# Kernel optimization log

Hardware: AMD Instinct MI355X
Metric: run time of the kernel (lower is better)

Reference implementation:

```python
import jax, jax.numpy as jnp
import numpy as np

# Config derived from init_kwargs
DIM = 256
DSTATE = 64
DCONV = 3
HEADDIM = 64
CHUNK = 256
NGROUPS = 1
DINNER = int(2.0 * DIM)                 # 512
NHEADS = DINNER // HEADDIM              # 8
CONVDIM = DINNER + 2 * NGROUPS * DSTATE  # 640 (x, B, C share the depthwise conv)
DPROJ = 2 * DINNER + 2 * NGROUPS * DSTATE + NHEADS  # z + xBC + dt


def setup_inputs() -> dict:
    key = jax.random.key(0)
    ks = jax.random.split(key, 8)
    B, H, W = 8, 64, 64
    return dict(
        x=jax.random.normal(ks[0], (B, DIM, H, W), jnp.float32),
        ln_w=jnp.ones((DIM,), jnp.float32),
        ln_b=jnp.zeros((DIM,), jnp.float32),
        in_proj_w=jax.random.normal(ks[1], (DPROJ, DIM), jnp.float32) * 0.02,
        conv_w=jax.random.normal(ks[2], (CONVDIM, 1, DCONV, DCONV), jnp.float32) * 0.1,
        conv_b=jnp.zeros((CONVDIM,), jnp.float32),
        A_log=jnp.log(jax.random.uniform(ks[3], (NHEADS,), jnp.float32, 1.0, 16.0)),
        D=jnp.ones((NHEADS,), jnp.float32),
        dt_bias=jax.random.uniform(ks[4], (NHEADS,), jnp.float32, -2.0, 0.0),
        rms_w=jnp.ones((DINNER,), jnp.float32),
        out_proj_w=jax.random.normal(ks[5], (DIM, DINNER), jnp.float32) * 0.02,
    )


def _ssd(X, dA, Bm, Cm, chunk):
    """Mamba2 SSD chunked parallel scan.
    X:  (b, l, h, p)  inputs already multiplied by dt
    dA: (b, l, h)     dt * A (negative)
    Bm, Cm: (b, l, h, n)
    """
    b, l, h, p = X.shape
    n = Bm.shape[-1]
    c = l // chunk
    q = chunk
    Xc = X.reshape(b, c, q, h, p)
    Bc = Bm.reshape(b, c, q, h, n)
    Cc = Cm.reshape(b, c, q, h, n)
    Ac = dA.reshape(b, c, q, h).transpose(0, 3, 1, 2)            # (b,h,c,q)
    Acs = jnp.cumsum(Ac, axis=-1)                                # (b,h,c,q)
    # intra-chunk (diagonal blocks): causal decay matrix L
    tri = jnp.tril(jnp.ones((q, q), bool))
    Ldec = jnp.where(tri, jnp.exp(Acs[..., :, None] - Acs[..., None, :]), 0.0)
    Y_diag = jnp.einsum('bcqhn,bcshn,bhcqs,bcshp->bcqhp', Cc, Bc, Ldec, Xc)
    # per-chunk final states
    decay_states = jnp.exp(Acs[..., -1:] - Acs)                  # (b,h,c,q)
    states = jnp.einsum('bcqhn,bhcq,bcqhp->bchpn', Bc, decay_states, Xc)
    # inter-chunk recurrence (segment-sum over chunk totals)
    A_last = jnp.pad(Acs[..., -1], ((0, 0), (0, 0), (1, 0)))     # (b,h,c+1)
    ccs = jnp.cumsum(A_last, axis=-1)
    tric = jnp.tril(jnp.ones((c + 1, c + 1), bool))
    decay_chunk = jnp.where(tric, jnp.exp(ccs[..., :, None] - ccs[..., None, :]), 0.0)
    states0 = jnp.concatenate([jnp.zeros_like(states[:, :1]), states], axis=1)
    prev = jnp.einsum('bhzc,bchpn->bzhpn', decay_chunk, states0)[:, :-1]
    # contribution of carried-in state (off-diagonal blocks)
    Y_off = jnp.einsum('bcqhn,bchpn,bhcq->bcqhp', Cc, prev, jnp.exp(Acs))
    return (Y_diag + Y_off).reshape(b, l, h, p)


def _forward(x, ln_w, ln_b, in_proj_w, conv_w, conv_b, A_log, D, dt_bias, rms_w, out_proj_w):
    Bn, Cd, Hh, Ww = x.shape
    L = Hh * Ww
    # LayerNorm over channel dim (channel-first LayerNorm2d)
    mu = jnp.mean(x, axis=1, keepdims=True)
    var = jnp.mean((x - mu) ** 2, axis=1, keepdims=True)
    xn = (x - mu) * jax.lax.rsqrt(var + 1e-5)
    xn = xn * ln_w[None, :, None, None] + ln_b[None, :, None, None]
    # input projection (1x1): -> z | xBC | dt
    zxbcdt = jnp.einsum('bchw,dc->bdhw', xn, in_proj_w)
    z = zxbcdt[:, :DINNER]
    xBC = zxbcdt[:, DINNER:DINNER + CONVDIM]
    dt = zxbcdt[:, DINNER + CONVDIM:]                            # (b, nheads, H, W)
    # depthwise 2D conv + SiLU on xBC
    xBC = jax.lax.conv_general_dilated(
        xBC, conv_w, (1, 1), 'SAME',
        dimension_numbers=('NCHW', 'OIHW', 'NCHW'), feature_group_count=CONVDIM)
    xBC = jax.nn.silu(xBC + conv_b[None, :, None, None])
    # flatten spatial -> sequence, channel-last
    def to_seq(t):
        return t.reshape(Bn, t.shape[1], L).transpose(0, 2, 1)
    xBC, dt, z = to_seq(xBC), to_seq(dt), to_seq(z)
    xs = xBC[..., :DINNER].reshape(Bn, L, NHEADS, HEADDIM)
    Bg = xBC[..., DINNER:DINNER + NGROUPS * DSTATE].reshape(Bn, L, NGROUPS, DSTATE)
    Cg = xBC[..., DINNER + NGROUPS * DSTATE:].reshape(Bn, L, NGROUPS, DSTATE)
    hpg = NHEADS // NGROUPS
    Bm = jnp.repeat(Bg, hpg, axis=2)
    Cm = jnp.repeat(Cg, hpg, axis=2)
    dt = jax.nn.softplus(dt + dt_bias[None, None, :])            # (b, L, nheads)
    A = -jnp.exp(A_log)
    y = _ssd(xs * dt[..., None], dt * A[None, None, :], Bm, Cm, CHUNK)
    y = y + D[None, None, :, None] * xs                          # skip connection
    y = y.reshape(Bn, L, DINNER)
    # gated RMSNorm: norm(y * silu(z)) * w
    y = y * jax.nn.silu(z)
    y = y * jax.lax.rsqrt(jnp.mean(y * y, axis=-1, keepdims=True) + 1e-5) * rms_w
    out = jnp.einsum('bld,cd->blc', y, out_proj_w)
    out = out.transpose(0, 2, 1).reshape(Bn, Cd, Hh, Ww)
    return x + out                                               # residual


def reference(x, ln_w, ln_b, in_proj_w, conv_w, conv_b, A_log, D, dt_bias, rms_w, out_proj_w):
    return _forward(x, ln_w, ln_b, in_proj_w, conv_w, conv_b, A_log, D, dt_bias, rms_w, out_proj_w)
```

## Files before the change

kernel.cpp:

```cpp
#include <hip/hip_runtime.h>
#include <hip/hip_bf16.h>
#include <math.h>

#define DIMC   256
#define LSP    4096
#define BATCH  8
#define DINNER 512
#define NHEADS 8
#define HEADDIM 64
#define DSTATE 64
#define CONVDIM 640
#define DPROJ  1160
#define MPAD   1280
#define CHUNK  256
#define NCHUNK 16

typedef unsigned short u16;
typedef __attribute__((ext_vector_type(8))) unsigned short u16x8;
typedef __attribute__((ext_vector_type(8))) short s16x8;
typedef __attribute__((ext_vector_type(4))) float f32x4;

#define MFMA16(a,b,c) __builtin_amdgcn_mfma_f32_16x16x32_bf16((s16x8)(a),(s16x8)(b),(c),0,0,0)

__device__ __forceinline__ float bf2f(u16 u){ return __uint_as_float(((unsigned int)u)<<16); }
__device__ __forceinline__ u16 f2bf(float f){
  unsigned int x = __float_as_uint(f);
  unsigned int r = (x + 0x7fffu + ((x>>16)&1u)) >> 16;
  return (u16)r;
}
__device__ __forceinline__ float softplusf(float x){ return (x > 20.f) ? x : __logf(1.f + __expf(x)); }
__device__ __forceinline__ float siluf(float x){ return x * __builtin_amdgcn_rcpf(1.f + __expf(-x)); }

__global__ void convert_w(const float* __restrict__ src, u16* __restrict__ dst,
                          int total, int valid){
  int i = blockIdx.x*256 + threadIdx.x;
  if (i >= total) return;
  dst[i] = (i < valid) ? f2bf(src[i]) : (u16)0;
}

__global__ void convert_w_rms(const float* __restrict__ src, const float* __restrict__ rmsw,
                              u16* __restrict__ dst){
  int i = blockIdx.x*256 + threadIdx.x;
  if (i >= DIMC*DINNER) return;
  dst[i] = f2bf(src[i] * rmsw[i & (DINNER-1)]);
}

__global__ void ln_kernel(const float* __restrict__ X, const float* __restrict__ lnw,
                          const float* __restrict__ lnb, u16* __restrict__ XNT) {
  int pos = blockIdx.x*256 + threadIdx.x;
  int b = pos >> 12, l = pos & (LSP-1);
  const float* xb = X + ((size_t)b*DIMC)*LSP + l;
  float sum=0.f, sq=0.f;
  for (int c=0;c<DIMC;c++){ float v=xb[(size_t)c*LSP]; sum+=v; sq+=v*v; }
  float mu = sum*(1.f/DIMC);
  float var = sq*(1.f/DIMC) - mu*mu;
  float rs = rsqrtf(var + 1e-5f);
  u16* ob = XNT + ((size_t)(b*LSP + l))*DIMC;
  for (int c0=0;c0<DIMC;c0+=8){
    u16x8 v8;
    #pragma unroll
    for(int j=0;j<8;j++){
      float v = xb[(size_t)(c0+j)*LSP];
      v8[j] = f2bf((v-mu)*rs*lnw[c0+j] + lnb[c0+j]);
    }
    *(u16x8*)&ob[c0] = v8;
  }
}

__global__ __launch_bounds__(256,2) void gemm_in_fused(
    const u16* __restrict__ W, const u16* __restrict__ XNT,
    u16* __restrict__ ZT, u16* __restrict__ XBC, u16* __restrict__ DT){
  __shared__ u16 Xs[128][264];
  __shared__ u16 Ws[128][32];
  int tid=threadIdx.x, w=tid>>6, lane=tid&63, l15=lane&15, quad=lane>>4;
  int n0=blockIdx.x*128, mh=blockIdx.y, b=blockIdx.z;
  {
    const u16* src = XNT + ((size_t)(b*LSP + n0))*DIMC;
    #pragma unroll
    for (int i=0;i<16;i++){
      int g = i*256 + tid;
      int row = g>>5, c8 = (g&31)*8;
      *(u16x8*)&Xs[row][c8] = *(const u16x8*)&src[(size_t)row*DIMC + c8];
    }
  }
  for (int pti=0; pti<5; pti++){
    int ptg = mh*5 + pti;
    int m0 = ptg*128;
    f32x4 acc[4][4];
    #pragma unroll
    for(int i=0;i<4;i++)
      #pragma unroll
      for(int j=0;j<4;j++) acc[i][j]=(f32x4){0.f,0.f,0.f,0.f};
    for (int k0=0;k0<DIMC;k0+=32){
      __syncthreads();
      {
        int ch = tid*2;
        int r = ch>>2, o=(ch&3)*8;
        *(u16x8*)&Ws[r][o] = *(const u16x8*)&W[(size_t)(m0+r)*DIMC + k0 + o];
        ch++; r = ch>>2; o=(ch&3)*8;
        *(u16x8*)&Ws[r][o] = *(const u16x8*)&W[(size_t)(m0+r)*DIMC + k0 + o];
      }
      __syncthreads();
      u16x8 af[4], bfr[4];
      if (ptg < 4){
        #pragma unroll
        for(int mt=0;mt<4;mt++) af[mt] = *(const u16x8*)&Xs[(w>>1)*64+mt*16+l15][k0+quad*8];
        #pragma unroll
        for(int nt=0;nt<4;nt++) bfr[nt] = *(const u16x8*)&Ws[(w&1)*64+nt*16+l15][quad*8];
      } else {
        #pragma unroll
        for(int mt=0;mt<4;mt++) af[mt] = *(const u16x8*)&Ws[(w>>1)*64+mt*16+l15][quad*8];
        #pragma unroll
        for(int nt=0;nt<4;nt++) bfr[nt] = *(const u16x8*)&Xs[(w&1)*64+nt*16+l15][k0+quad*8];
      }
      #pragma unroll
      for(int mt=0;mt<4;mt++)
        #pragma unroll
        for(int nt=0;nt<4;nt++)
          acc[mt][nt]=MFMA16(af[mt],bfr[nt],acc[mt][nt]);
    }
    if (ptg < 4){
      #pragma unroll
      for(int mt=0;mt<4;mt++)
        #pragma unroll
        for(int nt=0;nt<4;nt++)
          #pragma unroll
          for(int r=0;r<4;r++){
            int lrow = n0 + (w>>1)*64 + mt*16 + quad*4 + r;
            int dcol = m0 + (w&1)*64 + nt*16 + l15;
            ZT[((size_t)b*LSP + lrow)*DINNER + dcol] = f2bf(acc[mt][nt][r]);
          }
    } else {
      #pragma unroll
      for(int mt=0;mt<4;mt++)
        #pragma unroll
        for(int nt=0;nt<4;nt++)
          #pragma unroll
          for(int r=0;r<4;r++){
            int prow = m0 + (w>>1)*64 + mt*16 + quad*4 + r;
            if (prow>=DPROJ) continue;
            int col = n0 + (w&1)*64 + nt*16 + l15;
            u16 v = f2bf(acc[mt][nt][r]);
            if (prow<DINNER+CONVDIM)  XBC[((size_t)b*CONVDIM+(prow-DINNER))*LSP+col]=v;
            else                      DT[((size_t)b*NHEADS+(prow-DINNER-CONVDIM))*LSP+col]=v;
          }
    }
  }
}

__global__ void gemm_out_mfma(const u16* __restrict__ A, const u16* __restrict__ Bm,
                              const float* __restrict__ Res, float* __restrict__ Out){
  __shared__ u16 As[128][32];
  __shared__ u16 Bs[128][32];
  __shared__ float rinv[128];
  int tid=threadIdx.x, w=tid>>6, lane=tid&63, l15=lane&15, quad=lane>>4;
  int b=blockIdx.z, m0=blockIdx.y*128, n0=blockIdx.x*128;
  const u16* Bb = Bm + ((size_t)b*LSP + n0)*DINNER;
  f32x4 acc[4][4];
  #pragma unroll
  for(int i=0;i<4;i++)
    #pragma unroll
    for(int j=0;j<4;j++) acc[i][j] = (f32x4){0.f,0.f,0.f,0.f};
  float sqacc = 0.f;
  for (int k0=0;k0<DINNER;k0+=32){
    __syncthreads();
    {
      int ch = tid*2;
      int r = ch>>2, o=(ch&3)*8;
      *(u16x8*)&As[r][o] = *(const u16x8*)&A[(size_t)(m0+r)*DINNER + k0 + o];
      u16x8 bv = *(const u16x8*)&Bb[(size_t)r*DINNER + k0 + o];
      *(u16x8*)&Bs[r][o] = bv;
      #pragma unroll
      for(int j=0;j<8;j++){ float f=bf2f(bv[j]); sqacc += f*f; }
      ch++; r = ch>>2; o=(ch&3)*8;
      *(u16x8*)&As[r][o] = *(const u16x8*)&A[(size_t)(m0+r)*DINNER + k0 + o];
      u16x8 bv2 = *(const u16x8*)&Bb[(size_t)r*DINNER + k0 + o];
      *(u16x8*)&Bs[r][o] = bv2;
      #pragma unroll
      for(int j=0;j<8;j++){ float f=bf2f(bv2[j]); sqacc += f*f; }
    }
    __syncthreads();
    u16x8 af[4], bfr[4];
    #pragma unroll
    for(int mt=0;mt<4;mt++) af[mt] = *(const u16x8*)&As[(w>>1)*64+mt*16+l15][quad*8];
    #pragma unroll
    for(int nt=0;nt<4;nt++) bfr[nt] = *(const u16x8*)&Bs[(w&1)*64+nt*16+l15][quad*8];
    #pragma unroll
    for(int mt=0;mt<4;mt++)
      #pragma unroll
      for(int nt=0;nt<4;nt++)
        acc[mt][nt]=MFMA16(af[mt],bfr[nt],acc[mt][nt]);
  }
  {
    float tot = sqacc + __shfl_xor(sqacc, 1, 64);
    if ((tid&1)==0) rinv[tid>>1] = rsqrtf(tot*(1.f/DINNER) + 1e-5f);
  }
  __syncthreads();
  #pragma unroll
  for(int mt=0;mt<4;mt++)
    #pragma unroll
    for(int nt=0;nt<4;nt++){
      float rv = rinv[(w&1)*64 + nt*16 + l15];
      #pragma unroll
      for(int r=0;r<4;r++){
        int row = m0 + (w>>1)*64 + mt*16 + quad*4 + r;
        int col = n0 + (w&1)*64 + nt*16 + l15;
        size_t oi = ((size_t)b*DIMC+row)*LSP+col;
        Out[oi] = acc[mt][nt][r]*rv + Res[oi];
      }
    }
}

__global__ void conv_kernel(u16* __restrict__ XBC, const float* __restrict__ CW,
                            const float* __restrict__ CB){
  int ch = blockIdx.x, b = blockIdx.y, tid = threadIdx.x;
  __shared__ float plane[66*66];
  u16* base = XBC + ((size_t)b*CONVDIM + ch)*LSP;
  for (int idx=tid; idx<66*66; idx+=256){
    int yy = idx/66 - 1, xx = idx%66 - 1;
    float v = 0.f;
    if (yy>=0 && yy<64 && xx>=0 && xx<64) v = bf2f(base[yy*64+xx]);
    plane[idx] = v;
  }
  float wg[9];
  #pragma unroll
  for (int t=0;t<9;t++) wg[t] = CW[ch*9+t];
  float bias = CB[ch];
  __syncthreads();
  for (int r=0;r<16;r++){
    int pix = tid + r*256;
    int y = pix>>6, x = pix&63;
    float s=0.f;
    #pragma unroll
    for(int dy=0;dy<3;dy++)
      #pragma unroll
      for(int dx=0;dx<3;dx++) s += plane[(y+dy)*66 + x+dx]*wg[dy*3+dx];
    base[pix] = f2bf(siluf(s + bias));
  }
}

__global__ void ssd_pre_kernel(const u16* __restrict__ DT, const float* __restrict__ A_log,
                               const float* __restrict__ dt_bias, float* __restrict__ ACS,
                               float* __restrict__ DTV, float* __restrict__ DASUM){
  int c=blockIdx.x, h=blockIdx.y, b=blockIdx.z, tid=threadIdx.x;
  __shared__ float acs[CHUNK];
  size_t base = ((size_t)b*NHEADS+h)*LSP + c*CHUNK + tid;
  float raw = bf2f(DT[base]);
  float dtv = softplusf(raw + dt_bias[h]);
  float Ah = -__expf(A_log[h]);
  acs[tid] = dtv*Ah;
  __syncthreads();
  for(int o=1;o<256;o<<=1){
    float add=(tid>=o)?acs[tid-o]:0.f;
    __syncthreads(); acs[tid]+=add; __syncthreads();
  }
  ACS[base] = acs[tid];
  DTV[base] = dtv;
  if (tid==CHUNK-1) DASUM[((size_t)b*NHEADS+h)*NCHUNK+c] = acs[tid];
}

__global__ __launch_bounds__(256,4) void ssd_states_mfma(
    const float* __restrict__ ACS, const float* __restrict__ DTV,
    const float* __restrict__ DASUM, const u16* __restrict__ XBC,
    float* __restrict__ STATES){
  int c=blockIdx.x, h=blockIdx.y, b=blockIdx.z;
  int tid=threadIdx.x, w=tid>>6, lane=tid&63, l15=lane&15, quad=lane>>4;
  __shared__ float wdt[CHUNK];
  __shared__ u16 Xw[64][136];
  __shared__ u16 Bn[64][136];
  {
    size_t base = ((size_t)b*NHEADS+h)*LSP + c*CHUNK + tid;
    float atot = DASUM[((size_t)b*NHEADS+h)*NCHUNK+c];
    wdt[tid] = DTV[base]*__expf(atot - ACS[base]);
  }
  __syncthreads();
  f32x4 acc[4];
  #pragma unroll
  for(int i=0;i<4;i++) acc[i] = (f32x4){0.f,0.f,0.f,0.f};
  size_t cb = (size_t)c*CHUNK;
  for(int th=0; th<2; th++){
    __syncthreads();
    {
      int n=tid&63, q4=tid>>6;
      const u16* Xg = XBC + ((size_t)b*CONVDIM + h*HEADDIM + n)*LSP + cb + th*128;
      const u16* Bg = XBC + ((size_t)b*CONVDIM + DINNER + n)*LSP + cb + th*128;
      #pragma unroll
      for(int i=0;i<4;i++){
        int o = q4*32+i*8;
        u16x8 v = *(const u16x8*)&Xg[o];
        u16x8 wv;
        #pragma unroll
        for(int j=0;j<8;j++) wv[j]=f2bf(bf2f(v[j])*wdt[th*128+o+j]);
        *(u16x8*)&Xw[n][o]=wv;
        *(u16x8*)&Bn[n][o] = *(const u16x8*)&Bg[o];
      }
    }
    __syncthreads();
    #pragma unroll
    for(int k8=0;k8<4;k8++){
      u16x8 a = *(const u16x8*)&Xw[w*16+l15][k8*32+quad*8];
      #pragma unroll
      for(int nt=0;nt<4;nt++){
        u16x8 bb = *(const u16x8*)&Bn[nt*16+l15][k8*32+quad*8];
        acc[nt]=MFMA16(a,bb,acc[nt]);
      }
    }
  }
  float* dst = STATES + (((size_t)b*NHEADS+h)*NCHUNK+c)*4096;
  #pragma unroll
  for(int nt=0;nt<4;nt++)
    #pragma unroll
    for(int r=0;r<4;r++)
      dst[(w*16+quad*4+r)*64 + nt*16+l15] = acc[nt][r];
}

__global__ void ssd_scan_kernel(const float* __restrict__ STATES, const float* __restrict__ DASUM,
                                u16* __restrict__ PREVB){
  int g = blockIdx.x, h = blockIdx.y, b = blockIdx.z, tid = threadIdx.x;
  int e = g*256 + tid;
  size_t hb = (size_t)b*NHEADS + h;
  size_t base = hb*NCHUNK*4096 + e;
  float s = 0.f;
  for (int cc=0;cc<NCHUNK;cc++){
    PREVB[base + (size_t)cc*4096] = f2bf(s);
    s = s*__expf(DASUM[hb*NCHUNK + cc]) + STATES[base + (size_t)cc*4096];
  }
}

__global__ __launch_bounds__(256,7) void ssd_y_mfma(
    const float* __restrict__ ACS, const float* __restrict__ DTV,
    const u16* __restrict__ XBC, const float* __restrict__ Dp,
    const u16* __restrict__ PREVB, const u16* __restrict__ ZT,
    u16* __restrict__ YG){
  int h = blockIdx.x, bx = blockIdx.y, b = blockIdx.z;
  int c = bx>>2, tb = 3-(bx&3);
  int tid=threadIdx.x, w=tid>>6, lane=tid&63, l15=lane&15, quad=lane>>4;
  __shared__ float acs[CHUNK];
  __shared__ float dtv[CHUNK];
  __shared__ u16 BP[64][72];
  __shared__ u16 Xsb[64][72];
  {
    size_t base = ((size_t)b*NHEADS+h)*LSP + c*CHUNK + tid;
    acs[tid] = ACS[base];
    dtv[tid] = DTV[base];
  }
  u16x8 ca0, ca1;
  {
    const u16* Cbase = XBC + ((size_t)b*CONVDIM + DINNER + DSTATE)*LSP
                     + (size_t)c*CHUNK + tb*64 + w*16 + l15;
    #pragma unroll
    for(int j=0;j<8;j++){
      ca0[j] = Cbase[(size_t)(quad*8+j)*LSP];
      ca1[j] = Cbase[(size_t)(32+quad*8+j)*LSP];
    }
  }
  __syncthreads();
  f32x4 Yd[4], Yo[4];
  #pragma unroll
  for(int i=0;i<4;i++){ Yd[i]=(f32x4){0.f,0.f,0.f,0.f}; Yo[i]=(f32x4){0.f,0.f,0.f,0.f}; }
  {
    const u16* Pg = PREVB + (((size_t)b*NHEADS+h)*NCHUNK + c)*4096;
    #pragma unroll
    for(int pt=0;pt<4;pt++){
      u16x8 b0 = *(const u16x8*)&Pg[(pt*16+l15)*64 + quad*8];
      u16x8 b1 = *(const u16x8*)&Pg[(pt*16+l15)*64 + 32 + quad*8];
      Yo[pt]=MFMA16(ca0,b0,Yo[pt]);
      Yo[pt]=MFMA16(ca1,b1,Yo[pt]);
    }
  }
  int tloc = tb*64 + w*16 + quad*4;
  float acst[4];
  #pragma unroll
  for(int r=0;r<4;r++) acst[r] = acs[tloc+r];
  float Dh = Dp[h];
  for(int sb=0; sb<=tb; sb++){
    __syncthreads();
    {
      int n=tid&63, q4=tid>>6;
      const u16* Bg = XBC + ((size_t)b*CONVDIM + DINNER + n)*LSP + (size_t)c*CHUNK + sb*64;
      #pragma unroll
      for(int i=0;i<2;i++){
        u16x8 v = *(const u16x8*)&Bg[q4*16+i*8];
        #pragma unroll
        for(int j=0;j<8;j++) BP[q4*16+i*8+j][n]=v[j];
      }
      const u16* Xg = XBC + ((size_t)b*CONVDIM + h*HEADDIM + n)*LSP + (size_t)c*CHUNK + sb*64;
      #pragma unroll
      for(int i=0;i<2;i++){
        int o = q4*16+i*8;
        *(u16x8*)&Xsb[n][o] = *(const u16x8*)&Xg[o];
      }
    }
    __syncthreads();
    f32x4 S[4];
    #pragma unroll
    for(int st=0;st<4;st++){
      S[st]=(f32x4){0.f,0.f,0.f,0.f};
      u16x8 b0 = *(const u16x8*)&BP[st*16+l15][quad*8];
      u16x8 b1 = *(const u16x8*)&BP[st*16+l15][32+quad*8];
      S[st]=MFMA16(ca0,b0,S[st]);
      S[st]=MFMA16(ca1,b1,S[st]);
    }
    __syncthreads();
    if (sb < tb){
      #pragma unroll
      for(int st=0;st<4;st++){
        int s = sb*64 + st*16 + l15;
        float as = acs[s], dv = dtv[s];
        #pragma unroll
        for(int r=0;r<4;r++)
          BP[w*16+quad*4+r][st*16+l15] = f2bf(S[st][r]*__expf(acst[r]-as)*dv);
      }
    } else {
      #pragma unroll
      for(int st=0;st<4;st++){
        int s = sb*64 + st*16 + l15;
        float as = acs[s], dv = dtv[s];
        #pragma unroll
        for(int r=0;r<4;r++){
          int t = tloc + r;
          float pv;
          if (s < t)       pv = S[st][r]*__expf(acst[r]-as)*dv;
          else if (s == t) pv = S[st][r]*dv + Dh;
          else             pv = 0.f;
          BP[w*16+quad*4+r][st*16+l15] = f2bf(pv);
        }
      }
    }
    u16x8 p0 = *(const u16x8*)&BP[w*16+l15][quad*8];
    u16x8 p1 = *(const u16x8*)&BP[w*16+l15][32+quad*8];
    #pragma unroll
    for(int pt=0;pt<4;pt++){
      u16x8 x0 = *(const u16x8*)&Xsb[pt*16+l15][quad*8];
      u16x8 x1 = *(const u16x8*)&Xsb[pt*16+l15][32+quad*8];
      Yd[pt]=MFMA16(p0,x0,Yd[pt]);
      Yd[pt]=MFMA16(p1,x1,Yd[pt]);
    }
  }
  float eat[4];
  #pragma unroll
  for(int r=0;r<4;r++) eat[r] = __expf(acst[r]);
  size_t lbase = (size_t)b*LSP + c*CHUNK + tb*64;
  #pragma unroll
  for(int pt=0;pt<4;pt++){
    #pragma unroll
    for(int r=0;r<4;r++){
      int tl = w*16 + quad*4 + r;
      int p = pt*16 + l15;
      float y = Yd[pt][r] + eat[r]*Yo[pt][r];
      size_t oi = (lbase + tl)*DINNER + h*HEADDIM + p;
      float zv = bf2f(ZT[oi]);
      YG[oi] = f2bf(y * siluf(zv));
    }
  }
}

extern "C" void kernel_launch(void* const* d_in, const int* in_sizes, int n_in,
                              void* d_out, int out_size, void* d_ws, size_t ws_size,
                              hipStream_t stream) {
  const float* x     = (const float*)d_in[0];
  const float* lnw   = (const float*)d_in[1];
  const float* lnb   = (const float*)d_in[2];
  const float* inpw  = (const float*)d_in[3];
  const float* convw = (const float*)d_in[4];
  const float* convb = (const float*)d_in[5];
  const float* alog  = (const float*)d_in[6];
  const float* Dp    = (const float*)d_in[7];
  const float* dtbi  = (const float*)d_in[8];
  const float* rmsw  = (const float*)d_in[9];
  const float* outw  = (const float*)d_in[10];
  float* out = (float*)d_out;

  char* ws = (char*)d_ws;
  size_t off = 0;
  auto alloc = [&](size_t bytes)->void*{ void* p = ws+off; off += (bytes+255)&~(size_t)255; return p; };
  u16*   WPIN   = (u16*)  alloc((size_t)MPAD*DIMC*2);
  u16*   WPOUT  = (u16*)  alloc((size_t)DIMC*DINNER*2);
  char*  RA     = (char*) alloc((size_t)BATCH*NHEADS*NCHUNK*4096*4);
  u16*   XNT    = (u16*)RA;
  float* STATES = (float*)RA;
  u16*   ZT     = (u16*)  alloc((size_t)BATCH*LSP*DINNER*2);
  u16*   XBC    = (u16*)  alloc((size_t)BATCH*CONVDIM*LSP*2);
  u16*   DTb    = (u16*)  alloc((size_t)BATCH*NHEADS*LSP*2);
  u16*   PREVB  = (u16*)  alloc((size_t)BATCH*NHEADS*NCHUNK*4096*2);
  float* DASUM  = (float*)alloc((size_t)BATCH*NHEADS*NCHUNK*4);
  float* ACS    = (float*)alloc((size_t)BATCH*NHEADS*LSP*4);
  float* DTV    = (float*)alloc((size_t)BATCH*NHEADS*LSP*4);
  u16*   YG     = (u16*)  alloc((size_t)BATCH*LSP*DINNER*2);

  convert_w<<<(MPAD*DIMC+255)/256,256,0,stream>>>(inpw, WPIN, MPAD*DIMC, DPROJ*DIMC);
  convert_w_rms<<<(DIMC*DINNER+255)/256,256,0,stream>>>(outw, rmsw, WPOUT);
  ln_kernel<<<dim3(BATCH*LSP/256),256,0,stream>>>(x,lnw,lnb,XNT);
  gemm_in_fused<<<dim3(LSP/128,2,BATCH),256,0,stream>>>(WPIN, XNT, ZT, XBC, DTb);
  conv_kernel<<<dim3(CONVDIM,BATCH),256,0,stream>>>(XBC, convw, convb);
  ssd_pre_kernel<<<dim3(NCHUNK,NHEADS,BATCH),256,0,stream>>>(DTb, alog, dtbi, ACS, DTV, DASUM);
  ssd_states_mfma<<<dim3(NCHUNK,NHEADS,BATCH),256,0,stream>>>(ACS,DTV,DASUM,XBC,STATES);
  ssd_scan_kernel<<<dim3(16,NHEADS,BATCH),256,0,stream>>>(STATES,DASUM,PREVB);
  ssd_y_mfma<<<dim3(NHEADS,NCHUNK*4,BATCH),256,0,stream>>>(ACS,DTV,XBC,Dp,PREVB,ZT,YG);
  gemm_out_mfma<<<dim3(LSP/128,DIMC/128,BATCH),256,0,stream>>>(WPOUT, YG, x, out);
}
```

Before: 346.9 us.

## Process two heads per block in SSD output kernel with vectorized epilogue

Each ssd_y_mfma block now handles two heads, so the shared B/C score matrix (C·B^T) and the C and B tile loads are computed once and reused for both heads, halving the grid. The separate P buffer removes one barrier per sub-block. The epilogue stages Y in shared memory and writes YG with 16-byte vector loads and stores, where before each element was a scattered scalar access. In exchange, register and LDS use roughly double, so launch bounds drop to 3 blocks per CU and there are fewer blocks to hide latency.

After: 318.8 us. -8.1%, faster.

```diff
diff --git a/kernel.cpp b/kernel.cpp
--- a/kernel.cpp
+++ b/kernel.cpp
@@ -327,22 +327,26 @@
   }
 }
 
-__global__ __launch_bounds__(256,7) void ssd_y_mfma(
+__global__ __launch_bounds__(256,3) void ssd_y_mfma(
     const float* __restrict__ ACS, const float* __restrict__ DTV,
     const u16* __restrict__ XBC, const float* __restrict__ Dp,
     const u16* __restrict__ PREVB, const u16* __restrict__ ZT,
     u16* __restrict__ YG){
-  int h = blockIdx.x, bx = blockIdx.y, b = blockIdx.z;
+  int hp = blockIdx.x, bx = blockIdx.y, b = blockIdx.z;
+  int h0 = hp*2;
   int c = bx>>2, tb = 3-(bx&3);
   int tid=threadIdx.x, w=tid>>6, lane=tid&63, l15=lane&15, quad=lane>>4;
-  __shared__ float acs[CHUNK];
-  __shared__ float dtv[CHUNK];
-  __shared__ u16 BP[64][72];
-  __shared__ u16 Xsb[64][72];
-  {
-    size_t base = ((size_t)b*NHEADS+h)*LSP + c*CHUNK + tid;
-    acs[tid] = ACS[base];
-    dtv[tid] = DTV[base];
+  __shared__ float acs2[2][CHUNK];
+  __shared__ float dtv2[2][CHUNK];
+  __shared__ u16 Bs[64][72];
+  __shared__ u16 Xs[2][64][72];
+  __shared__ u16 Ps[2][64][72];
+  {
+    size_t base0 = ((size_t)b*NHEADS+h0)*LSP + c*CHUNK + tid;
+    acs2[0][tid] = ACS[base0];
+    dtv2[0][tid] = DTV[base0];
+    acs2[1][tid] = ACS[base0 + LSP];
+    dtv2[1][tid] = DTV[base0 + LSP];
   }
   u16x8 ca0, ca1;
   {
@@ -355,24 +359,29 @@
     }
   }
   __syncthreads();
-  f32x4 Yd[4], Yo[4];
-  #pragma unroll
-  for(int i=0;i<4;i++){ Yd[i]=(f32x4){0.f,0.f,0.f,0.f}; Yo[i]=(f32x4){0.f,0.f,0.f,0.f}; }
-  {
-    const u16* Pg = PREVB + (((size_t)b*NHEADS+h)*NCHUNK + c)*4096;
+  f32x4 Yd[2][4], Yo[2][4];
+  #pragma unroll
+  for(int hh=0;hh<2;hh++)
+    #pragma unroll
+    for(int i=0;i<4;i++){ Yd[hh][i]=(f32x4){0.f,0.f,0.f,0.f}; Yo[hh][i]=(f32x4){0.f,0.f,0.f,0.f}; }
+  #pragma unroll
+  for(int hh=0;hh<2;hh++){
+    const u16* Pg = PREVB + (((size_t)b*NHEADS+h0+hh)*NCHUNK + c)*4096;
     #pragma unroll
     for(int pt=0;pt<4;pt++){
       u16x8 b0 = *(const u16x8*)&Pg[(pt*16+l15)*64 + quad*8];
       u16x8 b1 = *(const u16x8*)&Pg[(pt*16+l15)*64 + 32 + quad*8];
-      Yo[pt]=MFMA16(ca0,b0,Yo[pt]);
-      Yo[pt]=MFMA16(ca1,b1,Yo[pt]);
+      Yo[hh][pt]=MFMA16(ca0,b0,Yo[hh][pt]);
+      Yo[hh][pt]=MFMA16(ca1,b1,Yo[hh][pt]);
     }
   }
   int tloc = tb*64 + w*16 + quad*4;
-  float acst[4];
-  #pragma unroll
-  for(int r=0;r<4;r++) acst[r] = acs[tloc+r];
-  float Dh = Dp[h];
+  float acst[2][4];
+  #pragma unroll
+  for(int hh=0;hh<2;hh++)
+    #pragma unroll
+    for(int r=0;r<4;r++) acst[hh][r] = acs2[hh][tloc+r];
+  float DhA[2] = { Dp[h0], Dp[h0+1] };
   for(int sb=0; sb<=tb; sb++){
     __syncthreads();
     {
@@ -382,13 +391,16 @@
       for(int i=0;i<2;i++){
         u16x8 v = *(const u16x8*)&Bg[q4*16+i*8];
         #pragma unroll
-        for(int j=0;j<8;j++) BP[q4*16+i*8+j][n]=v[j];
-      }
-      const u16* Xg = XBC + ((size_t)b*CONVDIM + h*HEADDIM + n)*LSP + (size_t)c*CHUNK + sb*64;
-      #pragma unroll
-      for(int i=0;i<2;i++){
-        int o = q4*16+i*8;
-        *(u16x8*)&Xsb[n][o] = *(const u16x8*)&Xg[o];
+        for(int j=0;j<8;j++) Bs[q4*16+i*8+j][n]=v[j];
+      }
+      #pragma unroll
+      for(int hh=0;hh<2;hh++){
+        const u16* Xg = XBC + ((size_t)b*CONVDIM + (h0+hh)*HEADDIM + n)*LSP + (size_t)c*CHUNK + sb*64;
+        #pragma unroll
+        for(int i=0;i<2;i++){
+          int o = q4*16+i*8;
+          *(u16x8*)&Xs[hh][n][o] = *(const u16x8*)&Xg[o];
+        }
       }
     }
     __syncthreads();
@@ -396,61 +408,85 @@
     #pragma unroll
     for(int st=0;st<4;st++){
       S[st]=(f32x4){0.f,0.f,0.f,0.f};
-      u16x8 b0 = *(const u16x8*)&BP[st*16+l15][quad*8];
-      u16x8 b1 = *(const u16x8*)&BP[st*16+l15][32+quad*8];
+      u16x8 b0 = *(const u16x8*)&Bs[st*16+l15][quad*8];
+      u16x8 b1 = *(const u16x8*)&Bs[st*16+l15][32+quad*8];
       S[st]=MFMA16(ca0,b0,S[st]);
       S[st]=MFMA16(ca1,b1,S[st]);
     }
-    __syncthreads();
-    if (sb < tb){
-      #pragma unroll
-      for(int st=0;st<4;st++){
-        int s = sb*64 + st*16 + l15;
-        float as = acs[s], dv = dtv[s];
-        #pragma unroll
-        for(int r=0;r<4;r++)
-          BP[w*16+quad*4+r][st*16+l15] = f2bf(S[st][r]*__expf(acst[r]-as)*dv);
-      }
-    } else {
-      #pragma unroll
-      for(int st=0;st<4;st++){
-        int s = sb*64 + st*16 + l15;
-        float as = acs[s], dv = dtv[s];
-        #pragma unroll
-        for(int r=0;r<4;r++){
-          int t = tloc + r;
-          float pv;
-          if (s < t)       pv = S[st][r]*__expf(acst[r]-as)*dv;
-          else if (s == t) pv = S[st][r]*dv + Dh;
-          else             pv = 0.f;
-          BP[w*16+quad*4+r][st*16+l15] = f2bf(pv);
+    #pragma unroll
+    for(int hh=0;hh<2;hh++){
+      float Dh = DhA[hh];
+      if (sb < tb){
+        #pragma unroll
+        for(int st=0;st<4;st++){
+          int s = sb*64 + st*16 + l15;
+          float as = acs2[hh][s], dv = dtv2[hh][s];
+          #pragma unroll
+          for(int r=0;r<4;r++)
+            Ps[hh][w*16+quad*4+r][st*16+l15] = f2bf(S[st][r]*__expf(acst[hh][r]-as)*dv);
         }
-      }
-    }
-    u16x8 p0 = *(const u16x8*)&BP[w*16+l15][quad*8];
-    u16x8 p1 = *(const u16x8*)&BP[w*16+l15][32+quad*8];
-    #pragma unroll
-    for(int pt=0;pt<4;pt++){
-      u16x8 x0 = *(const u16x8*)&Xsb[pt*16+l15][quad*8];
-      u16x8 x1 = *(const u16x8*)&Xsb[pt*16+l15][32+quad*8];
-      Yd[pt]=MFMA16(p0,x0,Yd[pt]);
-      Yd[pt]=MFMA16(p1,x1,Yd[pt]);
-    }
-  }
-  float eat[4];
-  #pragma unroll
-  for(int r=0;r<4;r++) eat[r] = __expf(acst[r]);
-  size_t lbase = (size_t)b*LSP + c*CHUNK + tb*64;
-  #pragma unroll
-  for(int pt=0;pt<4;pt++){
-    #pragma unroll
-    for(int r=0;r<4;r++){
-      int tl = w*16 + quad*4 + r;
-      int p = pt*16 + l15;
-      float y = Yd[pt][r] + eat[r]*Yo[pt][r];
-      size_t oi = (lbase + tl)*DINNER + h*HEADDIM + p;
-      float zv = bf2f(ZT[oi]);
-      YG[oi] = f2bf(y * siluf(zv));
+      } else {
+        #pragma unroll
+        for(int st=0;st<4;st++){
+          int s = sb*64 + st*16 + l15;
+          float as = acs2[hh][s], dv = dtv2[hh][s];
+          #pragma unroll
+          for(int r=0;r<4;r++){
+            int t = tloc + r;
+            float pv;
+            if (s < t)       pv = S[st][r]*__expf(acst[hh][r]-as)*dv;
+            else if (s == t) pv = S[st][r]*dv + Dh;
+            else             pv = 0.f;
+            Ps[hh][w*16+quad*4+r][st*16+l15] = f2bf(pv);
+          }
+        }
+      }
+      u16x8 p0 = *(const u16x8*)&Ps[hh][w*16+l15][quad*8];
+      u16x8 p1 = *(const u16x8*)&Ps[hh][w*16+l15][32+quad*8];
+      #pragma unroll
+      for(int pt=0;pt<4;pt++){
+        u16x8 x0 = *(const u16x8*)&Xs[hh][pt*16+l15][quad*8];
+        u16x8 x1 = *(const u16x8*)&Xs[hh][pt*16+l15][32+quad*8];
+        Yd[hh][pt]=MFMA16(p0,x0,Yd[hh][pt]);
+        Yd[hh][pt]=MFMA16(p1,x1,Yd[hh][pt]);
+      }
+    }
+  }
+  __syncthreads();
+  typedef float f32row[66];
+  f32row* Yf0 = (f32row*)Ps;
+  f32row* Yf1 = (f32row*)Xs;
+  {
+    float eat0[4], eat1[4];
+    #pragma unroll
+    for(int r=0;r<4;r++){ eat0[r]=__expf(acst[0][r]); eat1[r]=__expf(acst[1][r]); }
+    #pragma unroll
+    for(int pt=0;pt<4;pt++)
+      #pragma unroll
+      for(int r=0;r<4;r++){
+        int row = w*16 + quad*4 + r;
+        Yf0[row][pt*16+l15] = Yd[0][pt][r] + eat0[r]*Yo[0][pt][r];
+        Yf1[row][pt*16+l15] = Yd[1][pt][r] + eat1[r]*Yo[1][pt][r];
+      }
+  }
+  __syncthreads();
+  {
+    int row = tid>>2, seg = tid&3;
+    size_t lrow = (size_t)b*LSP + (size_t)c*CHUNK + tb*64 + row;
+    #pragma unroll
+    for(int hh=0;hh<2;hh++){
+      f32row* Yf = hh ? Yf1 : Yf0;
+      size_t oi = lrow*DINNER + (size_t)(h0+hh)*HEADDIM + seg*16;
+      u16x8 z0 = *(const u16x8*)&ZT[oi];
+      u16x8 z1 = *(const u16x8*)&ZT[oi+8];
+      u16x8 o0, o1;
+      #pragma unroll
+      for(int j=0;j<8;j++){
+        o0[j] = f2bf(Yf[row][seg*16+j]   * siluf(bf2f(z0[j])));
+        o1[j] = f2bf(Yf[row][seg*16+8+j] * siluf(bf2f(z1[j])));
+      }
+      *(u16x8*)&YG[oi]   = o0;
+      *(u16x8*)&YG[oi+8] = o1;
     }
   }
 }
@@ -496,6 +532,6 @@
   ssd_pre_kernel<<<dim3(NCHUNK,NHEADS,BATCH),256,0,stream>>>(DTb, alog, dtbi, ACS, DTV, DASUM);
   ssd_states_mfma<<<dim3(NCHUNK,NHEADS,BATCH),256,0,stream>>>(ACS,DTV,DASUM,XBC,STATES);
   ssd_scan_kernel<<<dim3(16,NHEADS,BATCH),256,0,stream>>>(STATES,DASUM,PREVB);
-  ssd_y_mfma<<<dim3(NHEADS,NCHUNK*4,BATCH),256,0,stream>>>(ACS,DTV,XBC,Dp,PREVB,ZT,YG);
+  ssd_y_mfma<<<dim3(NHEADS/2,NCHUNK*4,BATCH),256,0,stream>>>(ACS,DTV,XBC,Dp,PREVB,ZT,YG);
   gemm_out_mfma<<<dim3(LSP/128,DIMC/128,BATCH),256,0,stream>>>(WPOUT, YG, x, out);
 }
```
